# Optimization experiments

Hardware: AMD Instinct MI355X
Metric: run time of the kernel (lower is better)

The kernel has to match this reference:

```python
import jax, jax.numpy as jnp
import numpy as np

B, L, D_MODEL, H, DK, DV = 4, 2048, 1024, 16, 64, 64


def setup_inputs() -> dict:
    key = jax.random.key(0)
    ks = jax.random.split(key, 11)
    s = 1.0 / np.sqrt(D_MODEL)
    return {
        "queries": jax.random.normal(ks[0], (B, L, D_MODEL), jnp.float32),
        "keys": jax.random.normal(ks[1], (B, L, D_MODEL), jnp.float32),
        "values": jax.random.normal(ks[2], (B, L, D_MODEL), jnp.float32),
        "Wq": jax.random.normal(ks[3], (D_MODEL, H * DK), jnp.float32) * s,
        "bq": jnp.zeros((H * DK,), jnp.float32),
        "Wk": jax.random.normal(ks[4], (D_MODEL, H * DK), jnp.float32) * s,
        "bk": jnp.zeros((H * DK,), jnp.float32),
        "Wv": jax.random.normal(ks[5], (D_MODEL, H * DV), jnp.float32) * s,
        "bv": jnp.zeros((H * DV,), jnp.float32),
        "Wo": jax.random.normal(ks[6], (H * DV, D_MODEL), jnp.float32) * s,
        "bo": jnp.zeros((D_MODEL,), jnp.float32),
    }


def reference(queries, keys, values, Wq, bq, Wk, bk, Wv, bv, Wo, bo):
    b, l, _ = queries.shape
    s = keys.shape[1]
    q = (queries @ Wq + bq).reshape(b, l, H, DK)
    k = (keys @ Wk + bk).reshape(b, s, H, DK)
    v = (values @ Wv + bv).reshape(b, s, H, DV)
    scale = 1.0 / np.sqrt(DK)
    scores = jnp.einsum("blhe,bshe->bhls", q, k)  # [B,H,L,S]
    causal = jnp.triu(jnp.ones((l, s), bool), k=1)
    scores = jnp.where(causal[None, None], -jnp.inf, scores)
    A = jax.nn.softmax(scale * scores, axis=-1)
    out = jnp.einsum("bhls,bshd->blhd", A, v).reshape(b, l, H * DV)
    return out @ Wo + bo
```

## Files before the change

kernel.cpp:

```cpp
#include <hip/hip_runtime.h>

typedef __attribute__((ext_vector_type(8))) short s8v;
typedef __attribute__((ext_vector_type(4))) short s4v;
typedef __attribute__((ext_vector_type(4))) float f4v;
typedef __attribute__((ext_vector_type(4))) unsigned int u4v;

#define LOG2E 1.44269504088896340736f

__device__ __forceinline__ unsigned short f2bf(float f) {
    unsigned int x = __float_as_uint(f);
    return (unsigned short)((x + 0x7fffu + ((x >> 16) & 1u)) >> 16);
}
__device__ __forceinline__ s8v ld8(const unsigned short* p) {
    return *(const s8v*)p;
}

#define GLOAD_LDS(g, l) __builtin_amdgcn_global_load_lds(              \
    (const __attribute__((address_space(1))) void*)(const void*)(g),   \
    (__attribute__((address_space(3))) void*)(void*)(l), 16, 0, 0)

__global__ __launch_bounds__(256) void transpose_w4(
    const float* __restrict__ W0, const float* __restrict__ W1,
    const float* __restrict__ W2, const float* __restrict__ W3,
    unsigned short* __restrict__ T0, unsigned short* __restrict__ T1,
    unsigned short* __restrict__ T2, unsigned short* __restrict__ T3)
{
    __shared__ float tile[32][33];
    int z = blockIdx.z;
    const float* W = z == 0 ? W0 : z == 1 ? W1 : z == 2 ? W2 : W3;
    unsigned short* Wt = z == 0 ? T0 : z == 1 ? T1 : z == 2 ? T2 : T3;
    int tx = threadIdx.x, ty = threadIdx.y;
    int x = blockIdx.x * 32 + tx;
#pragma unroll
    for (int i = 0; i < 4; i++) {
        int y = blockIdx.y * 32 + ty + i * 8;
        tile[ty + i * 8][tx] = W[y * 1024 + x];
    }
    __syncthreads();
    int x2 = blockIdx.y * 32 + tx;
#pragma unroll
    for (int i = 0; i < 4; i++) {
        int y2 = blockIdx.x * 32 + ty + i * 8;
        Wt[y2 * 1024 + x2] = f2bf(tile[tx][ty + i * 8]);
    }
}

__global__ __launch_bounds__(256) void qkv_fused(
    const float* __restrict__ Aq, const float* __restrict__ Ak,
    const float* __restrict__ Avv,
    const unsigned short* __restrict__ BtQ, const unsigned short* __restrict__ BtK,
    const unsigned short* __restrict__ BtV,
    const float* __restrict__ bq, const float* __restrict__ bk,
    const float* __restrict__ bv,
    unsigned short* __restrict__ qo, unsigned short* __restrict__ ko,
    unsigned short* __restrict__ vo, float sscale)
{
    __shared__ __align__(16) unsigned short ldsA[3][128 * 32];
    __shared__ __align__(16) unsigned short ldsB[3][128 * 32];

    int i = blockIdx.x;
    int z = i >> 9;
    int r = i & 511;
    int c = r & 7, j = r >> 3;
    int bx = j & 7, by = c * 8 + (j >> 3);

    const float* A = z == 0 ? Aq : z == 1 ? Ak : Avv;
    const unsigned short* Bt = z == 0 ? BtQ : z == 1 ? BtK : BtV;
    const float* bias = z == 0 ? bq : z == 1 ? bk : bv;
    unsigned short* out = z == 0 ? qo : z == 1 ? ko : vo;
    float oscale = z == 0 ? sscale : 1.0f;

    int tid = threadIdx.x;
    int w = tid >> 6, lane = tid & 63;
    int quad = lane >> 4, l15 = lane & 15;
    int wr = w >> 1, wc = w & 1;
    int m0 = by * 128, n0 = bx * 128;

    int r1 = tid >> 2, qp = tid & 3;
    int qs = (qp ^ (r1 & 3)) * 8;
    const unsigned short* gb1 = Bt + (size_t)(n0 + r1) * 1024 + qs;
    const unsigned short* gb2 = Bt + (size_t)(n0 + r1 + 64) * 1024 + qs;

    int arow = tid >> 1, ahalf = tid & 1;
    const float* ap = A + (size_t)(m0 + arow) * 1024 + ahalf * 16;
    int awb0 = arow * 64 + (((2 * ahalf)     ^ (arow & 3)) << 4);
    int awb1 = arow * 64 + (((2 * ahalf + 1) ^ (arow & 3)) << 4);

    f4v acc[4][4];
#pragma unroll
    for (int m = 0; m < 4; m++)
#pragma unroll
        for (int n = 0; n < 4; n++) { f4v zz = {0.f, 0.f, 0.f, 0.f}; acc[m][n] = zz; }

    auto stageB = [&](int buf, int k0) {
        GLOAD_LDS(gb1 + k0, &ldsB[buf][w * 512]);
        GLOAD_LDS(gb2 + k0, &ldsB[buf][2048 + w * 512]);
    };
    auto cvtwrA = [&](int buf, f4v a0, f4v a1, f4v a2, f4v a3) {
        unsigned int w0, w1, w2, w3, w4, w5, w6, w7;
        asm("v_cvt_pk_bf16_f32 %0, %1, %2" : "=v"(w0) : "v"(a0[0]), "v"(a0[1]));
        asm("v_cvt_pk_bf16_f32 %0, %1, %2" : "=v"(w1) : "v"(a0[2]), "v"(a0[3]));
        asm("v_cvt_pk_bf16_f32 %0, %1, %2" : "=v"(w2) : "v"(a1[0]), "v"(a1[1]));
        asm("v_cvt_pk_bf16_f32 %0, %1, %2" : "=v"(w3) : "v"(a1[2]), "v"(a1[3]));
        asm("v_cvt_pk_bf16_f32 %0, %1, %2" : "=v"(w4) : "v"(a2[0]), "v"(a2[1]));
        asm("v_cvt_pk_bf16_f32 %0, %1, %2" : "=v"(w5) : "v"(a2[2]), "v"(a2[3]));
        asm("v_cvt_pk_bf16_f32 %0, %1, %2" : "=v"(w6) : "v"(a3[0]), "v"(a3[1]));
        asm("v_cvt_pk_bf16_f32 %0, %1, %2" : "=v"(w7) : "v"(a3[2]), "v"(a3[3]));
        u4v lo; lo[0] = w0; lo[1] = w1; lo[2] = w2; lo[3] = w3;
        u4v hi; hi[0] = w4; hi[1] = w5; hi[2] = w6; hi[3] = w7;
        char* base = (char*)&ldsA[buf][0];
        *(u4v*)(base + awb0) = lo;
        *(u4v*)(base + awb1) = hi;
    };

    int xr = (l15 & 3) << 4;

    {
        f4v a0 = *(const f4v*)ap,       a1 = *(const f4v*)(ap + 4);
        f4v a2 = *(const f4v*)(ap + 8), a3 = *(const f4v*)(ap + 12);
        stageB(0, 0);
        stageB(1, 32);
        asm volatile("s_waitcnt vmcnt(2)" ::: "memory");
        cvtwrA(0, a0, a1, a2, a3);
        asm volatile("s_waitcnt lgkmcnt(0)" ::: "memory");
        asm volatile("s_barrier" ::: "memory");
    }

    int buf = 0;
    for (int t = 0; t < 32; t++) {
        if (t < 30) {
            int nb = buf + 2; if (nb >= 3) nb -= 3;
            stageB(nb, (t + 2) * 32);
        }
        f4v a0, a1, a2, a3;
        if (t < 31) {
            const float* an = ap + (t + 1) * 32;
            a0 = *(const f4v*)an;       a1 = *(const f4v*)(an + 4);
            a2 = *(const f4v*)(an + 8); a3 = *(const f4v*)(an + 12);
        }
        const char* ab = (const char*)&ldsA[buf][0];
        const char* bb = (const char*)&ldsB[buf][0];
        s8v af[4], bfr[4];
#pragma unroll
        for (int m = 0; m < 4; m++)
            af[m] = *(const s8v*)(ab + (wr * 64 + m * 16 + l15) * 64 + ((quad * 16) ^ xr));
#pragma unroll
        for (int n = 0; n < 4; n++)
            bfr[n] = *(const s8v*)(bb + (wc * 64 + n * 16 + l15) * 64 + ((quad * 16) ^ xr));
        __builtin_amdgcn_s_setprio(1);
#pragma unroll
        for (int m = 0; m < 4; m++)
#pragma unroll
            for (int n = 0; n < 4; n++)
                acc[m][n] = __builtin_amdgcn_mfma_f32_16x16x32_bf16(af[m], bfr[n], acc[m][n], 0, 0, 0);
        __builtin_amdgcn_s_setprio(0);
        if (t < 31) {
            if (t < 30) asm volatile("s_waitcnt vmcnt(2)" ::: "memory");
            else        asm volatile("s_waitcnt vmcnt(0)" ::: "memory");
            int nb1 = buf + 1; if (nb1 >= 3) nb1 -= 3;
            cvtwrA(nb1, a0, a1, a2, a3);
            asm volatile("s_waitcnt lgkmcnt(0)" ::: "memory");
            asm volatile("s_barrier" ::: "memory");
            __builtin_amdgcn_sched_barrier(0);
        }
        buf++; if (buf >= 3) buf = 0;
    }

#pragma unroll
    for (int n = 0; n < 4; n++) {
        int col = n0 + wc * 64 + n * 16 + l15;
        float bvf = bias[col];
        int hh = col >> 6, d = col & 63;
#pragma unroll
        for (int m = 0; m < 4; m++) {
#pragma unroll
            for (int r2 = 0; r2 < 4; r2++) {
                int row = m0 + wr * 64 + m * 16 + quad * 4 + r2;
                float v = (acc[m][n][r2] + bvf) * oscale;
                int bb2 = row >> 11, l = row & 2047;
                if (z != 2) {
                    out[(((size_t)bb2 * 16 + hh) * 2048 + l) * 64 + d] = f2bf(v);
                } else {
                    int jj = l & 63;
                    int s = ((jj & 0x0C) << 2) | ((jj & 0x02) << 2) |
                            ((jj & 0x30) >> 3) | (jj & 1);
                    int lp = (l & ~63) | s;
                    out[(((size_t)bb2 * 16 + hh) * 64 + d) * 2048 + lp] = f2bf(v);
                }
            }
        }
    }
}

__global__ __launch_bounds__(256) void gemm_ctd(
    const unsigned short* __restrict__ A,
    const unsigned short* __restrict__ Bt,
    const float* __restrict__ bias,
    float* __restrict__ out)
{
    __shared__ __align__(16) unsigned short ldsA[3][128 * 32];
    __shared__ __align__(16) unsigned short ldsB[3][128 * 32];

    int i = blockIdx.x;
    int c = i & 7, j = i >> 3;
    int bx = j & 7, by = c * 8 + (j >> 3);

    int tid = threadIdx.x;
    int w = tid >> 6, lane = tid & 63;
    int quad = lane >> 4, l15 = lane & 15;
    int wr = w >> 1, wc = w & 1;
    int m0 = by * 128, n0 = bx * 128;

    int r1 = tid >> 2, qp = tid & 3;
    int qs = (qp ^ (r1 & 3)) * 8;
    const unsigned short* ga1 = A  + (size_t)(m0 + r1) * 1024 + qs;
    const unsigned short* ga2 = A  + (size_t)(m0 + r1 + 64) * 1024 + qs;
    const unsigned short* gb1 = Bt + (size_t)(n0 + r1) * 1024 + qs;
    const unsigned short* gb2 = Bt + (size_t)(n0 + r1 + 64) * 1024 + qs;

    f4v acc[4][4];
#pragma unroll
    for (int m = 0; m < 4; m++)
#pragma unroll
        for (int n = 0; n < 4; n++) { f4v zz = {0.f, 0.f, 0.f, 0.f}; acc[m][n] = zz; }

    auto stage = [&](int buf, int k0) {
        GLOAD_LDS(ga1 + k0, &ldsA[buf][w * 512]);
        GLOAD_LDS(ga2 + k0, &ldsA[buf][2048 + w * 512]);
        GLOAD_LDS(gb1 + k0, &ldsB[buf][w * 512]);
        GLOAD_LDS(gb2 + k0, &ldsB[buf][2048 + w * 512]);
    };

    int xr = (l15 & 3) << 4;

    stage(0, 0);
    stage(1, 32);
    asm volatile("s_waitcnt vmcnt(4)" ::: "memory");
    asm volatile("s_barrier" ::: "memory");

    int buf = 0;
    for (int t = 0; t < 32; t++) {
        if (t < 30) {
            int nb = buf + 2; if (nb >= 3) nb -= 3;
            stage(nb, (t + 2) * 32);
        }
        const char* ab = (const char*)&ldsA[buf][0];
        const char* bb = (const char*)&ldsB[buf][0];
        s8v af[4], bfr[4];
#pragma unroll
        for (int m = 0; m < 4; m++)
            af[m] = *(const s8v*)(ab + (wr * 64 + m * 16 + l15) * 64 + ((quad * 16) ^ xr));
#pragma unroll
        for (int n = 0; n < 4; n++)
            bfr[n] = *(const s8v*)(bb + (wc * 64 + n * 16 + l15) * 64 + ((quad * 16) ^ xr));
        __builtin_amdgcn_s_setprio(1);
#pragma unroll
        for (int m = 0; m < 4; m++)
#pragma unroll
            for (int n = 0; n < 4; n++)
                acc[m][n] = __builtin_amdgcn_mfma_f32_16x16x32_bf16(af[m], bfr[n], acc[m][n], 0, 0, 0);
        __builtin_amdgcn_s_setprio(0);
        if (t < 31) {
            if (t < 30) asm volatile("s_waitcnt vmcnt(4)" ::: "memory");
            else        asm volatile("s_waitcnt vmcnt(0)" ::: "memory");
            asm volatile("s_barrier" ::: "memory");
            __builtin_amdgcn_sched_barrier(0);
        }
        buf++; if (buf >= 3) buf = 0;
    }

#pragma unroll
    for (int n = 0; n < 4; n++) {
        int col = n0 + wc * 64 + n * 16 + l15;
        float bvf = bias[col];
#pragma unroll
        for (int m = 0; m < 4; m++)
#pragma unroll
            for (int r2 = 0; r2 < 4; r2++) {
                int row = m0 + wr * 64 + m * 16 + quad * 4 + r2;
                out[(size_t)row * 1024 + col] = acc[m][n][r2] + bvf;
            }
    }
}

__global__ __launch_bounds__(256) void attn_kernel(
    const unsigned short* __restrict__ Q,
    const unsigned short* __restrict__ K,
    const unsigned short* __restrict__ Vt,
    unsigned short* __restrict__ O)
{
    __shared__ __align__(16) unsigned short Kb[2][64 * 64];
    __shared__ __align__(16) unsigned short Vb[2][64 * 64];

    int tid = threadIdx.x;
    int w = tid >> 6, lane = tid & 63;
    int quad = lane >> 4, l15 = lane & 15;

    int bid = blockIdx.x;
    int swz = (bid & 7) * 128 + (bid >> 3);
    int xp = swz & 15;
    int h = (swz >> 4) & 15;
    int b = swz >> 8;
    int bh = b * 16 + h;

    int srow = tid >> 3;
    int soff = ((tid & 7) * 16) ^ ((srow & 7) << 4);
    const unsigned short* Kbase = K + (size_t)bh * 2048 * 64;
    const unsigned short* Vbase = Vt + (size_t)bh * 64 * 2048;

    auto stageK = [&](int buf, int kt) {
        const unsigned short* g1 = Kbase + (size_t)(kt * 64 + srow) * 64 + (soff >> 1);
        GLOAD_LDS(g1, &Kb[buf][w * 512]);
        GLOAD_LDS(g1 + (size_t)32 * 64, &Kb[buf][2048 + w * 512]);
    };
    auto stageV = [&](int buf, int kt) {
        const unsigned short* g1 = Vbase + (size_t)srow * 2048 + kt * 64 + (soff >> 1);
        GLOAD_LDS(g1, &Vb[buf][w * 512]);
        GLOAD_LDS(g1 + (size_t)32 * 2048, &Vb[buf][2048 + w * 512]);
    };

    int rswz = (l15 & 7) << 4;

#pragma unroll 1
    for (int half = 0; half < 2; half++) {
        int qt = half ? 31 - xp : xp;
        int m0 = qt * 64 + w * 16;

        const unsigned short* qb = Q + ((size_t)bh * 2048 + m0 + l15) * 64 + quad * 8;
        s8v aq0 = ld8(qb), aq1 = ld8(qb + 32);

        float mrun = -1e30f, lsum = 0.f;
        f4v oacc[4];
#pragma unroll
        for (int t = 0; t < 4; t++) { f4v z = {0.f, 0.f, 0.f, 0.f}; oacc[t] = z; }

        stageK(0, 0);
        stageV(0, 0);
        __syncthreads();

#pragma unroll 1
        for (int kt = 0; kt <= qt; kt++) {
            int buf = kt & 1;
            if (kt < qt) { stageK(buf ^ 1, kt + 1); stageV(buf ^ 1, kt + 1); }

            f4v sacc[4];
#pragma unroll
            for (int t = 0; t < 4; t++) { f4v z = {0.f, 0.f, 0.f, 0.f}; sacc[t] = z; }
            const char* kbp = (const char*)&Kb[buf][0];
#pragma unroll
            for (int t = 0; t < 4; t++) {
                int rb = (t * 16 + l15) * 128;
                s8v k0 = *(const s8v*)(kbp + rb + ((quad * 16) ^ rswz));
                s8v k1 = *(const s8v*)(kbp + rb + ((64 + quad * 16) ^ rswz));
                sacc[t] = __builtin_amdgcn_mfma_f32_16x16x32_bf16(k0, aq0, sacc[t], 0, 0, 0);
                sacc[t] = __builtin_amdgcn_mfma_f32_16x16x32_bf16(k1, aq1, sacc[t], 0, 0, 0);
            }

            if (kt == qt) {
                int qrow = w * 16 + l15;
#pragma unroll
                for (int t = 0; t < 4; t++)
#pragma unroll
                    for (int r = 0; r < 4; r++) {
                        int key = t * 16 + quad * 4 + r;
                        if (key > qrow) sacc[t][r] = -1e30f;
                    }
            }

            float tmax[4];
#pragma unroll
            for (int t = 0; t < 4; t++)
                tmax[t] = fmaxf(fmaxf(sacc[t][0], sacc[t][1]),
                                fmaxf(sacc[t][2], sacc[t][3]));
            float mx = fmaxf(fmaxf(tmax[0], tmax[1]), fmaxf(tmax[2], tmax[3]));
            mx = fmaxf(mx, __shfl_xor(mx, 16));
            mx = fmaxf(mx, __shfl_xor(mx, 32));

            if (__any(mx > mrun + 8.0f)) {
                float mnew = fmaxf(mrun, mx);
                float alpha = exp2f(mrun - mnew);
                lsum *= alpha;
#pragma unroll
                for (int r = 0; r < 4; r++) {
                    float ar = __shfl(alpha, quad * 4 + r);
#pragma unroll
                    for (int t2 = 0; t2 < 4; t2++) oacc[t2][r] *= ar;
                }
                mrun = mnew;
            }

            float ps[4];
#pragma unroll
            for (int t = 0; t < 4; t++) {
                float p0 = exp2f(sacc[t][0] - mrun);
                float p1 = exp2f(sacc[t][1] - mrun);
                float p2 = exp2f(sacc[t][2] - mrun);
                float p3 = exp2f(sacc[t][3] - mrun);
                sacc[t][0] = p0; sacc[t][1] = p1;
                sacc[t][2] = p2; sacc[t][3] = p3;
                ps[t] = (p0 + p1) + (p2 + p3);
            }
            lsum += (ps[0] + ps[1]) + (ps[2] + ps[3]);

            unsigned int pwv[4][2];
#pragma unroll
            for (int t = 0; t < 4; t++) {
                asm("v_cvt_pk_bf16_f32 %0, %1, %2"
                    : "=v"(pwv[t][0]) : "v"(sacc[t][0]), "v"(sacc[t][1]));
                asm("v_cvt_pk_bf16_f32 %0, %1, %2"
                    : "=v"(pwv[t][1]) : "v"(sacc[t][2]), "v"(sacc[t][3]));
            }

            const char* vbp = (const char*)&Vb[buf][0];
#pragma unroll
            for (int cc = 0; cc < 2; cc++) {
                u4v aw;
                aw[0] = pwv[0][cc]; aw[1] = pwv[1][cc];
                aw[2] = pwv[2][cc]; aw[3] = pwv[3][cc];
                s8v apf = __builtin_bit_cast(s8v, aw);
#pragma unroll
                for (int t2 = 0; t2 < 4; t2++) {
                    int rb = (t2 * 16 + l15) * 128;
                    s8v bvv = *(const s8v*)(vbp + rb + ((quad * 32 + cc * 16) ^ rswz));
                    oacc[t2] = __builtin_amdgcn_mfma_f32_16x16x32_bf16(apf, bvv, oacc[t2], 0, 0, 0);
                }
            }
            __syncthreads();
        }

        float ltot = lsum;
        ltot += __shfl_xor(ltot, 16);
        ltot += __shfl_xor(ltot, 32);
        float inv = 1.f / ltot;
#pragma unroll
        for (int r = 0; r < 4; r++) {
            float ir = __shfl(inv, quad * 4 + r);
            int l = m0 + quad * 4 + r;
#pragma unroll
            for (int t2 = 0; t2 < 4; t2++) {
                O[((size_t)b * 2048 + l) * 1024 + h * 64 + t2 * 16 + l15] = f2bf(oacc[t2][r] * ir);
            }
        }
    }
}

extern "C" void kernel_launch(void* const* d_in, const int* in_sizes, int n_in,
                              void* d_out, int out_size, void* d_ws, size_t ws_size,
                              hipStream_t stream)
{
    const float* queries = (const float*)d_in[0];
    const float* keys    = (const float*)d_in[1];
    const float* values  = (const float*)d_in[2];
    const float* Wq = (const float*)d_in[3];
    const float* bq = (const float*)d_in[4];
    const float* Wk = (const float*)d_in[5];
    const float* bk = (const float*)d_in[6];
    const float* Wv = (const float*)d_in[7];
    const float* bv = (const float*)d_in[8];
    const float* Wo = (const float*)d_in[9];
    const float* bo = (const float*)d_in[10];

    unsigned short* ws = (unsigned short*)d_ws;
    const size_t M1 = 1u << 20, M8 = 8u << 20;
    unsigned short* WqT = ws;
    unsigned short* WkT = ws + 1 * M1;
    unsigned short* WvT = ws + 2 * M1;
    unsigned short* WoT = ws + 3 * M1;
    unsigned short* qw  = ws + 4 * M1;
    unsigned short* kw  = qw + M8;
    unsigned short* vtw = kw + M8;
    unsigned short* ow  = vtw + M8;

    const float sscale = 0.125f * LOG2E;

    dim3 tb(32, 8);
    transpose_w4<<<dim3(32, 32, 4), tb, 0, stream>>>(
        Wq, Wk, Wv, Wo, WqT, WkT, WvT, WoT);

    qkv_fused<<<dim3(1536), 256, 0, stream>>>(
        queries, keys, values, WqT, WkT, WvT, bq, bk, bv,
        qw, kw, vtw, sscale);

    attn_kernel<<<dim3(1024), 256, 0, stream>>>(qw, kw, vtw, ow);

    gemm_ctd<<<dim3(512), 256, 0, stream>>>(ow, WoT, bo, (float*)d_out);
}
```

Measured before the change: 387.0 us.

## Rewrite QKV projection GEMM as 256x256 tile, 8-wave kernel with staged MFMA phases

Replaces the 128x128-tile, 4-wave, triple-buffered QKV projection GEMM with a 256x256-tile, 512-thread kernel that uses K-steps of 64, double buffering and an 8-way swizzle. Each k-step is split into four MFMA quadrants with interleaved LDS fragment loads and barriers, and the A-operand global loads and B-operand async copies are overlapped with compute. The larger tile is meant to cut global and LDS traffic per FLOP. In exchange, register pressure rises (32 accumulators), LDS use grows to 128 KB, and the grid shrinks to 384 blocks, which affects wave balance across CUs.

```diff
diff --git a/kernel.cpp b/kernel.cpp
--- a/kernel.cpp
+++ b/kernel.cpp
@@ -45,7 +45,31 @@
     }
 }
 
-__global__ __launch_bounds__(256) void qkv_fused(
+#define LOADA(MH)                                                             \
+    _Pragma("unroll") for (int m_ = 0; m_ < 4; m_++)                          \
+    _Pragma("unroll") for (int k_ = 0; k_ < 2; k_++)                          \
+        af[m_][k_] = *(const s8v*)(ab +                                       \
+            (wr * 128 + (MH) * 64 + m_ * 16 + l15) * 128 +                    \
+            ((k_ * 64 + quad * 16) ^ xsw));
+#define LOADB(NH)                                                             \
+    _Pragma("unroll") for (int n_ = 0; n_ < 2; n_++)                          \
+    _Pragma("unroll") for (int k_ = 0; k_ < 2; k_++)                          \
+        bfr[NH][n_][k_] = *(const s8v*)(bb +                                  \
+            (wc * 64 + (NH) * 32 + n_ * 16 + l15) * 128 +                     \
+            ((k_ * 64 + quad * 16) ^ xsw));
+#define MFMA16(MH, NH)                                                        \
+    _Pragma("unroll") for (int m_ = 0; m_ < 4; m_++)                          \
+    _Pragma("unroll") for (int n_ = 0; n_ < 2; n_++)                          \
+    _Pragma("unroll") for (int k_ = 0; k_ < 2; k_++)                          \
+        acc[((MH) * 4 + m_) * 4 + (NH) * 2 + n_] =                            \
+            __builtin_amdgcn_mfma_f32_16x16x32_bf16(af[m_][k_],               \
+                bfr[NH][n_][k_], acc[((MH) * 4 + m_) * 4 + (NH) * 2 + n_],    \
+                0, 0, 0);
+#define LGKM0 asm volatile("s_waitcnt lgkmcnt(0)" ::: "memory")
+#define SBAR  __builtin_amdgcn_s_barrier()
+#define SCHB  __builtin_amdgcn_sched_barrier(0)
+
+__global__ __launch_bounds__(512) void qkv8(
     const float* __restrict__ Aq, const float* __restrict__ Ak,
     const float* __restrict__ Avv,
     const unsigned short* __restrict__ BtQ, const unsigned short* __restrict__ BtK,
@@ -55,14 +79,14 @@
     unsigned short* __restrict__ qo, unsigned short* __restrict__ ko,
     unsigned short* __restrict__ vo, float sscale)
 {
-    __shared__ __align__(16) unsigned short ldsA[3][128 * 32];
-    __shared__ __align__(16) unsigned short ldsB[3][128 * 32];
+    __shared__ __align__(16) unsigned short ldsA[2][256 * 64];
+    __shared__ __align__(16) unsigned short ldsB[2][256 * 64];
 
     int i = blockIdx.x;
-    int z = i >> 9;
-    int r = i & 511;
-    int c = r & 7, j = r >> 3;
-    int bx = j & 7, by = c * 8 + (j >> 3);
+    int c = i & 7, j = i >> 3;
+    int p = j >> 2, bx = j & 3;
+    int zy = c * 12 + p;
+    int z = zy >> 5, by = zy & 31;
 
     const float* A = z == 0 ? Aq : z == 1 ? Ak : Avv;
     const unsigned short* Bt = z == 0 ? BtQ : z == 1 ? BtK : BtV;
@@ -70,123 +94,126 @@
     unsigned short* out = z == 0 ? qo : z == 1 ? ko : vo;
     float oscale = z == 0 ? sscale : 1.0f;
 
+    int m0 = by * 256, n0 = bx * 256;
     int tid = threadIdx.x;
     int w = tid >> 6, lane = tid & 63;
     int quad = lane >> 4, l15 = lane & 15;
-    int wr = w >> 1, wc = w & 1;
-    int m0 = by * 128, n0 = bx * 128;
-
-    int r1 = tid >> 2, qp = tid & 3;
-    int qs = (qp ^ (r1 & 3)) * 8;
-    const unsigned short* gb1 = Bt + (size_t)(n0 + r1) * 1024 + qs;
-    const unsigned short* gb2 = Bt + (size_t)(n0 + r1 + 64) * 1024 + qs;
-
+    int wr = w >> 2, wc = w & 3;
+    int xsw = (l15 & 7) << 4;
+
+    const unsigned short* srcB[4];
+#pragma unroll
+    for (int jj = 0; jj < 4; jj++) {
+        int ch = jj * 512 + tid;
+        int row = ch >> 3, sub = ch & 7;
+        srcB[jj] = Bt + (size_t)(n0 + row) * 1024 + (sub ^ (row & 7)) * 8;
+    }
     int arow = tid >> 1, ahalf = tid & 1;
-    const float* ap = A + (size_t)(m0 + arow) * 1024 + ahalf * 16;
-    int awb0 = arow * 64 + (((2 * ahalf)     ^ (arow & 3)) << 4);
-    int awb1 = arow * 64 + (((2 * ahalf + 1) ^ (arow & 3)) << 4);
-
-    f4v acc[4][4];
+    const float* apA = A + (size_t)(m0 + arow) * 1024 + ahalf * 32;
+    int wbyte[4];
+#pragma unroll
+    for (int q4 = 0; q4 < 4; q4++)
+        wbyte[q4] = arow * 128 + (((ahalf * 4 + q4) * 16) ^ ((arow & 7) << 4));
+
+    f4v acc[32];
+#pragma unroll
+    for (int a_ = 0; a_ < 32; a_++) { f4v zz = {0.f, 0.f, 0.f, 0.f}; acc[a_] = zz; }
+    s8v af[4][2];
+    s8v bfr[2][2][2];
+    f4v areg[8];
+
+    auto stageB = [&](int buf, int k0) {
+#pragma unroll
+        for (int jj = 0; jj < 4; jj++)
+            GLOAD_LDS(srcB[jj] + k0, &ldsB[buf][jj * 4096 + w * 512]);
+    };
+    auto issueA = [&](int kt) {
+        const float* an = apA + kt * 64;
+#pragma unroll
+        for (int jj = 0; jj < 8; jj++) areg[jj] = *(const f4v*)(an + jj * 4);
+    };
+    auto writeA = [&](int buf) {
+        char* base = (char*)&ldsA[buf][0];
+#pragma unroll
+        for (int q4 = 0; q4 < 4; q4++) {
+            unsigned int w0, w1, w2, w3;
+            asm("v_cvt_pk_bf16_f32 %0, %1, %2" : "=v"(w0)
+                : "v"(areg[2 * q4][0]), "v"(areg[2 * q4][1]));
+            asm("v_cvt_pk_bf16_f32 %0, %1, %2" : "=v"(w1)
+                : "v"(areg[2 * q4][2]), "v"(areg[2 * q4][3]));
+            asm("v_cvt_pk_bf16_f32 %0, %1, %2" : "=v"(w2)
+                : "v"(areg[2 * q4 + 1][0]), "v"(areg[2 * q4 + 1][1]));
+            asm("v_cvt_pk_bf16_f32 %0, %1, %2" : "=v"(w3)
+                : "v"(areg[2 * q4 + 1][2]), "v"(areg[2 * q4 + 1][3]));
+            u4v wv; wv[0] = w0; wv[1] = w1; wv[2] = w2; wv[3] = w3;
+            *(u4v*)(base + wbyte[q4]) = wv;
+        }
+    };
+
+    issueA(0);
+    stageB(0, 0);
+    stageB(1, 64);
+    asm volatile("s_waitcnt vmcnt(8)" ::: "memory");
+    SCHB;
+    writeA(0);
+    LGKM0;
+    asm volatile("s_waitcnt vmcnt(4)" ::: "memory");
+    SBAR;
+
+    for (int t = 0; t < 16; t++) {
+        const char* ab = (const char*)&ldsA[t & 1][0];
+        const char* bb = (const char*)&ldsB[t & 1][0];
+        LOADA(0)
+        LOADB(0)
+        if (t < 15) issueA(t + 1);
+        SBAR; LGKM0; SCHB;
+        __builtin_amdgcn_s_setprio(1); MFMA16(0, 0); __builtin_amdgcn_s_setprio(0);
+        SBAR;
+        LOADB(1)
+        SBAR; LGKM0; SCHB;
+        __builtin_amdgcn_s_setprio(1); MFMA16(0, 1); __builtin_amdgcn_s_setprio(0);
+        SBAR;
+        LOADA(1)
+        SBAR; LGKM0; SCHB;
+        __builtin_amdgcn_s_setprio(1); MFMA16(1, 0); __builtin_amdgcn_s_setprio(0);
+        SBAR;
+        if (t < 14) stageB(t & 1, (t + 2) * 64);
+        __builtin_amdgcn_s_setprio(1); MFMA16(1, 1); __builtin_amdgcn_s_setprio(0);
+        if (t < 15) {
+            if (t < 14) asm volatile("s_waitcnt vmcnt(4)" ::: "memory");
+            else        asm volatile("s_waitcnt vmcnt(0)" ::: "memory");
+            SCHB;
+            writeA((t + 1) & 1);
+            LGKM0;
+        }
+        SBAR;
+    }
+
+#pragma unroll
+    for (int mh = 0; mh < 2; mh++)
 #pragma unroll
     for (int m = 0; m < 4; m++)
 #pragma unroll
-        for (int n = 0; n < 4; n++) { f4v zz = {0.f, 0.f, 0.f, 0.f}; acc[m][n] = zz; }
-
-    auto stageB = [&](int buf, int k0) {
-        GLOAD_LDS(gb1 + k0, &ldsB[buf][w * 512]);
-        GLOAD_LDS(gb2 + k0, &ldsB[buf][2048 + w * 512]);
-    };
-    auto cvtwrA = [&](int buf, f4v a0, f4v a1, f4v a2, f4v a3) {
-        unsigned int w0, w1, w2, w3, w4, w5, w6, w7;
-        asm("v_cvt_pk_bf16_f32 %0, %1, %2" : "=v"(w0) : "v"(a0[0]), "v"(a0[1]));
-        asm("v_cvt_pk_bf16_f32 %0, %1, %2" : "=v"(w1) : "v"(a0[2]), "v"(a0[3]));
-        asm("v_cvt_pk_bf16_f32 %0, %1, %2" : "=v"(w2) : "v"(a1[0]), "v"(a1[1]));
-        asm("v_cvt_pk_bf16_f32 %0, %1, %2" : "=v"(w3) : "v"(a1[2]), "v"(a1[3]));
-        asm("v_cvt_pk_bf16_f32 %0, %1, %2" : "=v"(w4) : "v"(a2[0]), "v"(a2[1]));
-        asm("v_cvt_pk_bf16_f32 %0, %1, %2" : "=v"(w5) : "v"(a2[2]), "v"(a2[3]));
-        asm("v_cvt_pk_bf16_f32 %0, %1, %2" : "=v"(w6) : "v"(a3[0]), "v"(a3[1]));
-        asm("v_cvt_pk_bf16_f32 %0, %1, %2" : "=v"(w7) : "v"(a3[2]), "v"(a3[3]));
-        u4v lo; lo[0] = w0; lo[1] = w1; lo[2] = w2; lo[3] = w3;
-        u4v hi; hi[0] = w4; hi[1] = w5; hi[2] = w6; hi[3] = w7;
-        char* base = (char*)&ldsA[buf][0];
-        *(u4v*)(base + awb0) = lo;
-        *(u4v*)(base + awb1) = hi;
-    };
-
-    int xr = (l15 & 3) << 4;
-
-    {
-        f4v a0 = *(const f4v*)ap,       a1 = *(const f4v*)(ap + 4);
-        f4v a2 = *(const f4v*)(ap + 8), a3 = *(const f4v*)(ap + 12);
-        stageB(0, 0);
-        stageB(1, 32);
-        asm volatile("s_waitcnt vmcnt(2)" ::: "memory");
-        cvtwrA(0, a0, a1, a2, a3);
-        asm volatile("s_waitcnt lgkmcnt(0)" ::: "memory");
-        asm volatile("s_barrier" ::: "memory");
-    }
-
-    int buf = 0;
-    for (int t = 0; t < 32; t++) {
-        if (t < 30) {
-            int nb = buf + 2; if (nb >= 3) nb -= 3;
-            stageB(nb, (t + 2) * 32);
-        }
-        f4v a0, a1, a2, a3;
-        if (t < 31) {
-            const float* an = ap + (t + 1) * 32;
-            a0 = *(const f4v*)an;       a1 = *(const f4v*)(an + 4);
-            a2 = *(const f4v*)(an + 8); a3 = *(const f4v*)(an + 12);
-        }
-        const char* ab = (const char*)&ldsA[buf][0];
-        const char* bb = (const char*)&ldsB[buf][0];
-        s8v af[4], bfr[4];
-#pragma unroll
-        for (int m = 0; m < 4; m++)
-            af[m] = *(const s8v*)(ab + (wr * 64 + m * 16 + l15) * 64 + ((quad * 16) ^ xr));
-#pragma unroll
-        for (int n = 0; n < 4; n++)
-            bfr[n] = *(const s8v*)(bb + (wc * 64 + n * 16 + l15) * 64 + ((quad * 16) ^ xr));
-        __builtin_amdgcn_s_setprio(1);
-#pragma unroll
-        for (int m = 0; m < 4; m++)
-#pragma unroll
-            for (int n = 0; n < 4; n++)
-                acc[m][n] = __builtin_amdgcn_mfma_f32_16x16x32_bf16(af[m], bfr[n], acc[m][n], 0, 0, 0);
-        __builtin_amdgcn_s_setprio(0);
-        if (t < 31) {
-            if (t < 30) asm volatile("s_waitcnt vmcnt(2)" ::: "memory");
-            else        asm volatile("s_waitcnt vmcnt(0)" ::: "memory");
-            int nb1 = buf + 1; if (nb1 >= 3) nb1 -= 3;
-            cvtwrA(nb1, a0, a1, a2, a3);
-            asm volatile("s_waitcnt lgkmcnt(0)" ::: "memory");
-            asm volatile("s_barrier" ::: "memory");
-            __builtin_amdgcn_sched_barrier(0);
-        }
-        buf++; if (buf >= 3) buf = 0;
-    }
-
-#pragma unroll
-    for (int n = 0; n < 4; n++) {
-        int col = n0 + wc * 64 + n * 16 + l15;
+    for (int nh = 0; nh < 2; nh++)
+#pragma unroll
+    for (int n2 = 0; n2 < 2; n2++) {
+        f4v a = acc[(mh * 4 + m) * 4 + nh * 2 + n2];
+        int col = n0 + wc * 64 + nh * 32 + n2 * 16 + l15;
         float bvf = bias[col];
         int hh = col >> 6, d = col & 63;
 #pragma unroll
-        for (int m = 0; m < 4; m++) {
-#pragma unroll
-            for (int r2 = 0; r2 < 4; r2++) {
-                int row = m0 + wr * 64 + m * 16 + quad * 4 + r2;
-                float v = (acc[m][n][r2] + bvf) * oscale;
-                int bb2 = row >> 11, l = row & 2047;
-                if (z != 2) {
-                    out[(((size_t)bb2 * 16 + hh) * 2048 + l) * 64 + d] = f2bf(v);
-                } else {
-                    int jj = l & 63;
-                    int s = ((jj & 0x0C) << 2) | ((jj & 0x02) << 2) |
-                            ((jj & 0x30) >> 3) | (jj & 1);
-                    int lp = (l & ~63) | s;
-                    out[(((size_t)bb2 * 16 + hh) * 64 + d) * 2048 + lp] = f2bf(v);
-                }
+        for (int r = 0; r < 4; r++) {
+            int row = m0 + wr * 128 + mh * 64 + m * 16 + quad * 4 + r;
+            float v = (a[r] + bvf) * oscale;
+            int bb2 = row >> 11, l = row & 2047;
+            if (z != 2) {
+                out[(((size_t)bb2 * 16 + hh) * 2048 + l) * 64 + d] = f2bf(v);
+            } else {
+                int jj = l & 63;
+                int s = ((jj & 0x0C) << 2) | ((jj & 0x02) << 2) |
+                        ((jj & 0x30) >> 3) | (jj & 1);
+                int lp = (l & ~63) | s;
+                out[(((size_t)bb2 * 16 + hh) * 64 + d) * 2048 + lp] = f2bf(v);
             }
         }
     }
@@ -477,7 +504,7 @@
     transpose_w4<<<dim3(32, 32, 4), tb, 0, stream>>>(
         Wq, Wk, Wv, Wo, WqT, WkT, WvT, WoT);
 
-    qkv_fused<<<dim3(1536), 256, 0, stream>>>(
+    qkv8<<<dim3(384), 512, 0, stream>>>(
         queries, keys, values, WqT, WkT, WvT, bq, bk, bv,
         qw, kw, vtw, sscale);
 
```

Measured after the change: 422.7 us. +9.2%, slower.
